# Kernel optimization log

Hardware: AMD Instinct MI355X
Metric: run time of the kernel (lower is better)

Reference implementation:

```python
import jax, jax.numpy as jnp
import numpy as np

B, T, F, H = 32, 512, 32, 256
EPS = 1e-5

def _ln(x, g, b):
    m = jnp.mean(x, axis=-1, keepdims=True)
    v = jnp.var(x, axis=-1, keepdims=True)
    return (x - m) / jnp.sqrt(v + EPS) * g + b

def setup_inputs() -> dict:
    key = jax.random.key(0)
    ks = jax.random.split(key, 30)
    n = lambda k, shp, fan: jax.random.normal(k, shp, dtype=jnp.float32) / np.sqrt(fan)
    d = {}
    d['x'] = jax.random.normal(ks[0], (B, T, F), dtype=jnp.float32)
    # per-feature GRN params (stacked over F); in_dim=1 so fc1/skip weights are (F,H)
    d['w1'] = n(ks[1], (F, H), 1); d['b1'] = jnp.zeros((F, H), jnp.float32)
    d['w2'] = n(ks[2], (F, H, H), H); d['b2'] = jnp.zeros((F, H), jnp.float32)
    d['wg'] = n(ks[3], (F, H, H), H); d['bg'] = jnp.zeros((F, H), jnp.float32)
    d['wf'] = n(ks[4], (F, H, H), H); d['bf'] = jnp.zeros((F, H), jnp.float32)
    d['gamma'] = jnp.ones((F, H), jnp.float32); d['beta'] = jnp.zeros((F, H), jnp.float32)
    d['ws'] = n(ks[5], (F, H), 1); d['bs'] = jnp.zeros((F, H), jnp.float32)
    # selection GRN: in_dim=F*H, hidden=H, out=F
    FH = F * H
    d['sw1'] = n(ks[6], (FH, H), FH); d['sb1'] = jnp.zeros((H,), jnp.float32)
    d['sw2'] = n(ks[7], (H, F), H); d['sb2'] = jnp.zeros((F,), jnp.float32)
    d['swg'] = n(ks[8], (F, F), F); d['sbg'] = jnp.zeros((F,), jnp.float32)
    d['swf'] = n(ks[9], (F, F), F); d['sbf'] = jnp.zeros((F,), jnp.float32)
    d['sgamma'] = jnp.ones((F,), jnp.float32); d['sbeta'] = jnp.zeros((F,), jnp.float32)
    d['ssw'] = n(ks[10], (FH, F), FH); d['ssb'] = jnp.zeros((F,), jnp.float32)
    return d

def reference(x, w1, b1, w2, b2, wg, bg, wf, bf, gamma, beta, ws, bs,
              sw1, sb1, sw2, sb2, swg, sbg, swf, sbf, sgamma, sbeta, ssw, ssb):
    # --- per-feature GRNs, vectorized over the feature axis ---
    xe = x[..., None]                                   # (B,T,F,1)
    h = jax.nn.elu(xe * w1 + b1)                        # (B,T,F,H)
    h = jnp.einsum('btfh,fhk->btfk', h, w2) + b2        # fc2
    glu = jax.nn.sigmoid(jnp.einsum('btfh,fhk->btfk', h, wg) + bg) \
          * (jnp.einsum('btfh,fhk->btfk', h, wf) + bf)
    residual = xe * ws + bs                             # skip Linear(1,H)
    stacked = _ln(residual + glu, gamma, beta)          # (B,T,F,H)
    # --- selection GRN over flattened features ---
    flat = stacked.reshape(B, T, F * H)
    sh = jax.nn.elu(flat @ sw1 + sb1)                   # (B,T,H)
    sh = sh @ sw2 + sb2                                 # (B,T,F)
    sglu = jax.nn.sigmoid(sh @ swg + sbg) * (sh @ swf + sbf)
    sres = flat @ ssw + ssb
    weights = jax.nn.softmax(_ln(sres + sglu, sgamma, sbeta), axis=-1)  # (B,T,F)
    # --- weighted sum over features ---
    return jnp.einsum('btfh,btf->bth', stacked, weights)  # (B,T,H)
```

## Files before the change

### kernel.cpp

```cpp
#include <hip/hip_runtime.h>
#include <hip/hip_bf16.h>
#include <hip/hip_fp16.h>

#define BT 16384
#define F 32
#define H 256
#define FH 8192
#define SPLITK 4

typedef _Float16 half8 __attribute__((ext_vector_type(8)));
typedef _Float16 half4v __attribute__((ext_vector_type(4)));
typedef float float4v __attribute__((ext_vector_type(4)));

#define GLD_LDS(gsrc, ldst) \
    __builtin_amdgcn_global_load_lds( \
        (const __attribute__((address_space(1))) void*)(gsrc), \
        (__attribute__((address_space(3))) void*)(ldst), 16, 0, 0)

#define WAITVM2_BAR() do { \
    __builtin_amdgcn_sched_barrier(0); \
    asm volatile("s_waitcnt vmcnt(2)" ::: "memory"); \
    __builtin_amdgcn_s_barrier(); \
    __builtin_amdgcn_sched_barrier(0); } while (0)
#define WAITVM0_BAR() do { \
    __builtin_amdgcn_sched_barrier(0); \
    asm volatile("s_waitcnt vmcnt(0)" ::: "memory"); \
    __builtin_amdgcn_s_barrier(); \
    __builtin_amdgcn_sched_barrier(0); } while (0)
#define END_BAR() do { \
    __builtin_amdgcn_sched_barrier(0); \
    __builtin_amdgcn_s_barrier(); \
    __builtin_amdgcn_sched_barrier(0); } while (0)
#define LGKM_BAR() do { \
    __builtin_amdgcn_sched_barrier(0); \
    asm volatile("s_waitcnt lgkmcnt(0)" ::: "memory"); \
    __builtin_amdgcn_s_barrier(); \
    __builtin_amdgcn_sched_barrier(0); } while (0)

__global__ __launch_bounds__(256) void transpose_w_kernel(
    const float* __restrict__ w2, const float* __restrict__ wg,
    const float* __restrict__ wf, _Float16* __restrict__ wt)
{
    __shared__ float tile[64][65];
    int bid = blockIdx.x;
    int tens = bid >> 9, rem = bid & 511;
    int f = rem >> 4, tl = rem & 15;
    int hb = (tl >> 2) * 64, nb = (tl & 3) * 64;
    const float* src = (tens == 0 ? w2 : (tens == 1 ? wg : wf)) + f * 65536;
    _Float16* dst = wt + (size_t)tens * 2097152 + f * 65536;
    int lane = threadIdx.x & 63, w = threadIdx.x >> 6;
    for (int i = 0; i < 16; ++i) {
        int r = i * 4 + w;
        tile[r][lane] = src[(hb + r) * 256 + nb + lane];
    }
    __syncthreads();
    for (int i = 0; i < 16; ++i) {
        int c = i * 4 + w;
        dst[(nb + c) * 256 + hb + lane] = (_Float16)tile[lane][c];
    }
}

__global__ __launch_bounds__(256) void transpose_s_kernel(
    const float* __restrict__ sw1, const float* __restrict__ ssw,
    _Float16* __restrict__ wcat)
{
    __shared__ float tile[64][65];
    int bid = blockIdx.x;
    int lane = threadIdx.x & 63, w = threadIdx.x >> 6;
    if (bid < 512) {
        int k0 = (bid >> 2) * 64, n0 = (bid & 3) * 64;
        for (int i = 0; i < 16; ++i) {
            int r = i * 4 + w;
            tile[r][lane] = sw1[(size_t)(k0 + r) * 256 + n0 + lane];
        }
        __syncthreads();
        for (int i = 0; i < 16; ++i) {
            int c = i * 4 + w;
            wcat[(size_t)(n0 + c) * FH + k0 + lane] = (_Float16)tile[lane][c];
        }
    } else {
        int k0 = (bid - 512) * 64;
        int t = threadIdx.x;
        for (int i = 0; i < 8; ++i) {
            int idx = t + i * 256;
            int r = idx >> 5, cc = idx & 31;
            tile[r][cc] = ssw[(size_t)(k0 + r) * 32 + cc];
        }
        __syncthreads();
        for (int i = 0; i < 8; ++i) {
            int idx = t + i * 256;
            int c = idx >> 6, rr = idx & 63;
            wcat[(size_t)(256 + c) * FH + k0 + rr] = (_Float16)tile[rr][c];
        }
    }
}

__global__ __launch_bounds__(512, 4) void grn_kernel(
    const float* __restrict__ x, const float* __restrict__ w1, const float* __restrict__ b1,
    const float* __restrict__ b2, const float* __restrict__ bg, const float* __restrict__ bfv_,
    const float* __restrict__ gamma, const float* __restrict__ beta,
    const float* __restrict__ wsk, const float* __restrict__ bsk,
    const _Float16* __restrict__ w2t, const _Float16* __restrict__ wgt,
    const _Float16* __restrict__ wft, _Float16* __restrict__ stacked, int tok_base)
{
    __shared__ __align__(16) char smem[65536];
    _Float16* As = (_Float16*)smem;
    _Float16* Bs = (_Float16*)(smem + 32768);
    float* red = (float*)smem;
    float* mv  = (float*)(smem + 2048);

    const int bid = blockIdx.x;
    const int xcd = bid & 7;
    const int slot = bid >> 3;
    const int f = xcd * 4 + (slot & 3);
    const int tok0 = (slot >> 2) * 64;
    const int t = threadIdx.x;
    const int wv = t >> 6;
    const int ln = t & 15;
    const int q  = (t >> 4) & 3;
    const int wm = wv >> 2;
    const int wn = wv & 3;
    const int r0 = wm * 32 + ln;
    const int r1 = r0 + 16;

    const _Float16* w2f = w2t + (size_t)f * 65536;
    const _Float16* wgf = wgt + (size_t)f * 65536;
    const _Float16* wff = wft + (size_t)f * 65536;

#define GRN_STAGE(buf, Bsrc, kc) do {                                          \
        const _Float16* _bp = (Bsrc);                                          \
        _Pragma("unroll")                                                      \
        for (int _i = 0; _i < 2; ++_i) {                                       \
            int _s = t + _i * 512;                                             \
            int _row = _s >> 2;                                                \
            int _c = (_s & 3) ^ ((_row >> 1) & 3);                             \
            GLD_LDS(_bp + _row * 256 + (kc) * 32 + _c * 8,                     \
                    Bs + (buf) * 8192 + _s * 8);                               \
        } } while (0)

#define GRN_MFMA(ACC, kc) do {                                                 \
        const _Float16* _B = Bs + ((kc) & 1) * 8192;                           \
        half8 _a0 = *(const half8*)&As[r0 * 256 + ((((kc) * 4 + q) ^ (r0 & 7)) << 3)]; \
        half8 _a1 = *(const half8*)&As[r1 * 256 + ((((kc) * 4 + q) ^ (r1 & 7)) << 3)]; \
        _Pragma("unroll")                                                      \
        for (int _nt = 0; _nt < 4; ++_nt) {                                    \
            int _rb = wn * 64 + _nt * 16 + ln;                                 \
            int _cp = q ^ ((_rb >> 1) & 3);                                    \
            half8 _b8 = *(const half8*)&_B[_rb * 32 + _cp * 8];                \
            ACC[0][_nt] = __builtin_amdgcn_mfma_f32_16x16x32_f16(              \
                _a0, _b8, ACC[0][_nt], 0, 0, 0);                               \
            ACC[1][_nt] = __builtin_amdgcn_mfma_f32_16x16x32_f16(              \
                _a1, _b8, ACC[1][_nt], 0, 0, 0);                               \
        } } while (0)

    float b2v[4];
#pragma unroll
    for (int nt = 0; nt < 4; ++nt) b2v[nt] = b2[f * H + wn * 64 + nt * 16 + ln];

    GRN_STAGE(0, w2f, 0);

    {
        const int colE = t & 255;
        const int rgE = __builtin_amdgcn_readfirstlane(t >> 8) * 32;
        const float w1v = w1[f * H + colE];
        const float b1v = b1[f * H + colE];
        const int chE = colE >> 3, elE = colE & 7;
#pragma unroll 8
        for (int i = 0; i < 32; ++i) {
            int row = rgE + i;
            float xv = x[(size_t)(tok_base + tok0 + row) * F + f];
            float z = fmaf(xv, w1v, b1v);
            float e = z > 0.f ? z : (__expf(z) - 1.f);
            As[row * 256 + ((chE ^ (row & 7)) << 3) + elE] = (_Float16)e;
        }
    }
    LGKM_BAR();

    float4v acc1[2][4];
#pragma unroll
    for (int mt = 0; mt < 2; ++mt)
#pragma unroll
        for (int nt = 0; nt < 4; ++nt)
#pragma unroll
            for (int r = 0; r < 4; ++r) acc1[mt][nt][r] = 0.f;

#pragma unroll
    for (int kc = 0; kc < 8; ++kc) {
        if (kc < 7) GRN_STAGE((kc + 1) & 1, w2f, kc + 1);
        else        GRN_STAGE(0, wgf, 0);
        WAITVM2_BAR();
        GRN_MFMA(acc1, kc);
        END_BAR();
    }

    {
#pragma unroll
        for (int mt = 0; mt < 2; ++mt)
#pragma unroll
            for (int nt = 0; nt < 4; ++nt) {
                int n = wn * 64 + nt * 16 + ln;
#pragma unroll
                for (int r = 0; r < 4; ++r) {
                    int row = wm * 32 + mt * 16 + q * 4 + r;
                    As[row * 256 + (((n >> 3) ^ (row & 7)) << 3) + (n & 7)] =
                        (_Float16)(acc1[mt][nt][r] + b2v[nt]);
                }
            }
    }
    LGKM_BAR();

    float4v accG[2][4], accF[2][4];
#pragma unroll
    for (int mt = 0; mt < 2; ++mt)
#pragma unroll
        for (int nt = 0; nt < 4; ++nt)
#pragma unroll
            for (int r = 0; r < 4; ++r) { accG[mt][nt][r] = 0.f; accF[mt][nt][r] = 0.f; }

#pragma unroll
    for (int kc = 0; kc < 8; ++kc) {
        if (kc < 7) GRN_STAGE((kc + 1) & 1, wgf, kc + 1);
        else        GRN_STAGE(0, wff, 0);
        WAITVM2_BAR();
        GRN_MFMA(accG, kc);
        END_BAR();
    }
#pragma unroll
    for (int kc = 0; kc < 8; ++kc) {
        if (kc < 7) {
            GRN_STAGE((kc + 1) & 1, wff, kc + 1);
            WAITVM2_BAR();
        } else {
            WAITVM0_BAR();
        }
        GRN_MFMA(accF, kc);
        END_BAR();
    }
#undef GRN_STAGE
#undef GRN_MFMA

    float xr[2][4];
#pragma unroll
    for (int mt = 0; mt < 2; ++mt)
#pragma unroll
        for (int r = 0; r < 4; ++r)
            xr[mt][r] = x[(size_t)(tok_base + tok0 + wm * 32 + mt * 16 + q * 4 + r) * F + f];
#pragma unroll
    for (int nt = 0; nt < 4; ++nt) {
        int nn = f * H + wn * 64 + nt * 16 + ln;
        float bgv = bg[nn], bfv = bfv_[nn], wsv = wsk[nn], bsv = bsk[nn];
#pragma unroll
        for (int mt = 0; mt < 2; ++mt)
#pragma unroll
            for (int r = 0; r < 4; ++r) {
                float cg = accG[mt][nt][r] + bgv;
                float cf = accF[mt][nt][r] + bfv;
                float sig = 1.f / (1.f + __expf(-cg));
                accG[mt][nt][r] = sig * cf + xr[mt][r] * wsv + bsv;
            }
    }

#pragma unroll
    for (int mt = 0; mt < 2; ++mt)
#pragma unroll
        for (int r = 0; r < 4; ++r) {
            float v0 = accG[mt][0][r], v1 = accG[mt][1][r];
            float v2 = accG[mt][2][r], v3 = accG[mt][3][r];
            float s1 = (v0 + v1) + (v2 + v3);
            float s2 = (v0 * v0 + v1 * v1) + (v2 * v2 + v3 * v3);
#pragma unroll
            for (int m = 1; m <= 8; m <<= 1) {
                s1 += __shfl_xor(s1, m, 64);
                s2 += __shfl_xor(s2, m, 64);
            }
            if (ln == 0) {
                int row = wm * 32 + mt * 16 + q * 4 + r;
                red[row * 4 + wn] = s1;
                red[256 + row * 4 + wn] = s2;
            }
        }
    __syncthreads();
    if (t < 64) {
        float a = (red[t * 4] + red[t * 4 + 1]) + (red[t * 4 + 2] + red[t * 4 + 3]);
        float b = (red[256 + t * 4] + red[256 + t * 4 + 1])
                + (red[256 + t * 4 + 2] + red[256 + t * 4 + 3]);
        float mean = a * (1.f / 256.f);
        float var = b * (1.f / 256.f) - mean * mean;
        mv[t] = mean;
        mv[64 + t] = rsqrtf(var + 1e-5f);
    }
    __syncthreads();

    float mr[2][4], rr[2][4];
#pragma unroll
    for (int mt = 0; mt < 2; ++mt)
#pragma unroll
        for (int r = 0; r < 4; ++r) {
            int row = wm * 32 + mt * 16 + q * 4 + r;
            mr[mt][r] = mv[row];
            rr[mt][r] = mv[64 + row];
        }
#pragma unroll
    for (int nt = 0; nt < 4; ++nt) {
        int n = wn * 64 + nt * 16 + ln;
        float gv = gamma[f * H + n], bvv = beta[f * H + n];
#pragma unroll
        for (int mt = 0; mt < 2; ++mt)
#pragma unroll
            for (int r = 0; r < 4; ++r) {
                int row = wm * 32 + mt * 16 + q * 4 + r;
                float vv = (accG[mt][nt][r] - mr[mt][r]) * rr[mt][r] * gv + bvv;
                stacked[(size_t)(tok0 + row) * FH + f * H + n] = (_Float16)vv;
            }
    }
}

__global__ __launch_bounds__(256, 3) void sel_gemm_kernel(
    const _Float16* __restrict__ stacked, const _Float16* __restrict__ wcat,
    float* __restrict__ sh_part, float* __restrict__ sres_part, int C)
{
    __shared__ __align__(16) _Float16 As2[2][64 * 64];
    const int t = threadIdx.x;
    const int wv = t >> 6;
    const int ln = t & 15, q = (t & 63) >> 4;
    const int bid = blockIdx.x;
    const int xcd = bid & 7;
    const int slot = bid >> 3;
    const int kb = xcd >> 1;
    const int tok0 = (slot * 2 + (xcd & 1)) * 64;

    const int s1 = t + 256;
    const int row0 = t >> 3,  c0 = ((t & 7) ^ (row0 & 7)) * 8;
    const int row1 = s1 >> 3, c1 = ((s1 & 7) ^ (row1 & 7)) * 8;
    const _Float16* a0src = stacked + (size_t)(tok0 + row0) * FH + kb * 2048 + c0;
    const _Float16* a1src = stacked + (size_t)(tok0 + row1) * FH + kb * 2048 + c1;

    float4v acc[4][5];
#pragma unroll
    for (int mt = 0; mt < 4; ++mt)
#pragma unroll
        for (int i = 0; i < 5; ++i)
#pragma unroll
            for (int r = 0; r < 4; ++r) acc[mt][i][r] = 0.f;

    GLD_LDS(a0src, &As2[0][t * 8]);
    GLD_LDS(a1src, &As2[0][s1 * 8]);
    __syncthreads();

    for (int kc = 0; kc < 32; ++kc) {
        const int cur = kc & 1;
        half8 bb0[5], bb1[5];
#define SEL_LOAD(i)                                                            \
        {                                                                      \
            const _Float16* bp = wcat                                          \
                + (size_t)((wv + 4 * (i)) * 16 + ln) * FH                      \
                + kb * 2048 + kc * 64 + q * 8;                                 \
            bb0[i] = *(const half8*)bp;                                        \
            bb1[i] = *(const half8*)(bp + 32);                                 \
        }
        SEL_LOAD(0) SEL_LOAD(1) SEL_LOAD(2) SEL_LOAD(3)
        if (wv < 2) SEL_LOAD(4)
#undef SEL_LOAD
        if (kc < 31) {
            GLD_LDS(a0src + (kc + 1) * 64, &As2[cur ^ 1][t * 8]);
            GLD_LDS(a1src + (kc + 1) * 64, &As2[cur ^ 1][s1 * 8]);
        }
        const _Float16* As = As2[cur];
        half8 af0[4], af1[4];
#pragma unroll
        for (int mt = 0; mt < 4; ++mt) {
            int row = mt * 16 + ln;
            af0[mt] = *(const half8*)&As[row * 64 + ((q ^ (row & 7)) * 8)];
            af1[mt] = *(const half8*)&As[row * 64 + (((4 + q) ^ (row & 7)) * 8)];
        }
#define SEL_FMA(i)                                                            \
        {                                                                      \
            _Pragma("unroll")                                                  \
            for (int mt = 0; mt < 4; ++mt)                                     \
                acc[mt][i] = __builtin_amdgcn_mfma_f32_16x16x32_f16(           \
                    af0[mt], bb0[i], acc[mt][i], 0, 0, 0);                     \
            _Pragma("unroll")                                                  \
            for (int mt = 0; mt < 4; ++mt)                                     \
                acc[mt][i] = __builtin_amdgcn_mfma_f32_16x16x32_f16(           \
                    af1[mt], bb1[i], acc[mt][i], 0, 0, 0);                     \
        }
        SEL_FMA(0) SEL_FMA(1) SEL_FMA(2) SEL_FMA(3)
        if (wv < 2) SEL_FMA(4)
#undef SEL_FMA
        __syncthreads();
    }

    float* shp = sh_part + (size_t)kb * ((size_t)C * 256);
    float* srp = sres_part + (size_t)kb * ((size_t)C * 32);
#pragma unroll
    for (int i = 0; i < 4; ++i) {
        int n = (wv + 4 * i) * 16 + ln;
#pragma unroll
        for (int mt = 0; mt < 4; ++mt)
#pragma unroll
            for (int r = 0; r < 4; ++r) {
                int m = tok0 + mt * 16 + q * 4 + r;
                shp[(size_t)m * 256 + n] = acc[mt][i][r];
            }
    }
    if (wv < 2) {
        int n = wv * 16 + ln;
#pragma unroll
        for (int mt = 0; mt < 4; ++mt)
#pragma unroll
            for (int r = 0; r < 4; ++r) {
                int m = tok0 + mt * 16 + q * 4 + r;
                srp[(size_t)m * 32 + n] = acc[mt][4][r];
            }
    }
}

__global__ __launch_bounds__(256) void tail_kernel(
    const float* __restrict__ sh_part, const float* __restrict__ sres_part,
    const _Float16* __restrict__ stacked,
    const float* __restrict__ sb1, const float* __restrict__ ssb,
    const float* __restrict__ sw2, const float* __restrict__ sb2,
    const float* __restrict__ swg, const float* __restrict__ sbg,
    const float* __restrict__ swf, const float* __restrict__ sbf,
    const float* __restrict__ sgam, const float* __restrict__ sbet,
    float* __restrict__ out, int tok_base, int C)
{
    __shared__ float sw2s[256 * 32];
    __shared__ float swgs[1024], swfs[1024];
    __shared__ float shv[8][260];
    __shared__ float wls[8][33];
    const int t = threadIdx.x;
    const size_t shS = (size_t)C * 256;
    const size_t srS = (size_t)C * 32;
    for (int i = 0; i < 32; ++i) sw2s[t + i * 256] = sw2[t + i * 256];
    for (int i = 0; i < 4; ++i) {
        swgs[t + i * 256] = swg[t + i * 256];
        swfs[t + i * 256] = swf[t + i * 256];
    }
#pragma unroll
    for (int i = 0; i < 2; ++i) {
        int slot = t + i * 256;
        int gg = slot >> 6;
        int c4 = (slot & 63) * 4;
        size_t o = (size_t)(blockIdx.x * 8 + gg) * 256 + c4;
        float4v z = *(const float4v*)&sb1[c4];
        z += *(const float4v*)&sh_part[o];
        z += *(const float4v*)&sh_part[shS + o];
        z += *(const float4v*)&sh_part[2 * shS + o];
        z += *(const float4v*)&sh_part[3 * shS + o];
        float4v e;
#pragma unroll
        for (int j = 0; j < 4; ++j)
            e[j] = z[j] > 0.f ? z[j] : (__expf(z[j]) - 1.f);
        *(float4v*)&shv[gg][c4] = e;
    }
    __syncthreads();
    const int g = t >> 5;
    const int j = t & 31;
    const int token = blockIdx.x * 8 + g;
    float p = sb2[j];
    for (int k = 0; k < 256; ++k) p += shv[g][k] * sw2s[k * 32 + j];
    float gacc = sbg[j], uacc = sbf[j];
#pragma unroll 8
    for (int i = 0; i < 32; ++i) {
        float tv = __shfl(p, i, 32);
        gacc += tv * swgs[i * 32 + j];
        uacc += tv * swfs[i * 32 + j];
    }
    float sig = 1.f / (1.f + __expf(-gacc));
    size_t o2 = (size_t)token * 32 + j;
    float sresv = ssb[j] + sres_part[o2] + sres_part[srS + o2]
                + sres_part[2 * srS + o2] + sres_part[3 * srS + o2];
    float sv = sresv + sig * uacc;
    float s1 = sv, s2 = sv * sv;
    for (int off = 16; off; off >>= 1) {
        s1 += __shfl_xor(s1, off, 32);
        s2 += __shfl_xor(s2, off, 32);
    }
    float mean = s1 * (1.f / 32.f);
    float var = s2 * (1.f / 32.f) - mean * mean;
    float v = (sv - mean) * rsqrtf(var + 1e-5f) * sgam[j] + sbet[j];
    float mx = v;
    for (int off = 16; off; off >>= 1) mx = fmaxf(mx, __shfl_xor(mx, off, 32));
    float e = __expf(v - mx);
    float ssum = e;
    for (int off = 16; off; off >>= 1) ssum += __shfl_xor(ssum, off, 32);
    wls[g][j] = e / ssum;
    __syncthreads();
    {
        const int tg = t >> 6;
        const int c4 = (t & 63) * 4;
#pragma unroll
        for (int tt = 0; tt < 2; ++tt) {
            int tk = tg * 2 + tt;
            const _Float16* sp = stacked + (size_t)(blockIdx.x * 8 + tk) * FH;
            float a0 = 0.f, a1 = 0.f, a2 = 0.f, a3 = 0.f;
#pragma unroll
            for (int f = 0; f < 32; ++f) {
                half4v vv = *(const half4v*)&sp[f * 256 + c4];
                float w = wls[tk][f];
                a0 += (float)vv[0] * w;
                a1 += (float)vv[1] * w;
                a2 += (float)vv[2] * w;
                a3 += (float)vv[3] * w;
            }
            float4v ov; ov[0] = a0; ov[1] = a1; ov[2] = a2; ov[3] = a3;
            *(float4v*)&out[(size_t)(tok_base + blockIdx.x * 8 + tk) * 256 + c4] = ov;
        }
    }
}

extern "C" void kernel_launch(void* const* d_in, const int* in_sizes, int n_in,
                              void* d_out, int out_size, void* d_ws, size_t ws_size,
                              hipStream_t stream)
{
    (void)in_sizes; (void)n_in; (void)out_size;
    const float* x    = (const float*)d_in[0];
    const float* w1   = (const float*)d_in[1];
    const float* b1   = (const float*)d_in[2];
    const float* w2   = (const float*)d_in[3];
    const float* b2   = (const float*)d_in[4];
    const float* wg   = (const float*)d_in[5];
    const float* bg   = (const float*)d_in[6];
    const float* wf   = (const float*)d_in[7];
    const float* bfp  = (const float*)d_in[8];
    const float* gamma= (const float*)d_in[9];
    const float* beta = (const float*)d_in[10];
    const float* wsk  = (const float*)d_in[11];
    const float* bsk  = (const float*)d_in[12];
    const float* sw1  = (const float*)d_in[13];
    const float* sb1  = (const float*)d_in[14];
    const float* sw2  = (const float*)d_in[15];
    const float* sb2  = (const float*)d_in[16];
    const float* swg  = (const float*)d_in[17];
    const float* sbg  = (const float*)d_in[18];
    const float* swf  = (const float*)d_in[19];
    const float* sbf  = (const float*)d_in[20];
    const float* sgam = (const float*)d_in[21];
    const float* sbet = (const float*)d_in[22];
    const float* ssw  = (const float*)d_in[23];
    const float* ssb  = (const float*)d_in[24];

    const size_t fixedB = 12582912 + 4718592;
    int C = BT;
    while (C > 512) {
        size_t need = fixedB + (size_t)C * 20992;
        if (need <= ws_size) break;
        C >>= 1;
    }
    const int nChunks = BT / C;

    char* ws = (char*)d_ws;
    _Float16* wt      = (_Float16*)ws;
    _Float16* wcat    = (_Float16*)(ws + 12582912);
    char* p = ws + fixedB;
    _Float16* stacked = (_Float16*)p;            p += (size_t)C * FH * 2;
    float* sh_part    = (float*)p;               p += (size_t)C * 256 * 4 * SPLITK;
    float* sres_part  = (float*)p;
    float* out        = (float*)d_out;

    hipLaunchKernelGGL(transpose_w_kernel, dim3(1536), dim3(256), 0, stream, w2, wg, wf, wt);
    hipLaunchKernelGGL(transpose_s_kernel, dim3(640), dim3(256), 0, stream, sw1, ssw, wcat);
    for (int c = 0; c < nChunks; ++c) {
        int tb = c * C;
        hipLaunchKernelGGL(grn_kernel, dim3((C / 64) * 32), dim3(512), 0, stream,
                           x, w1, b1, b2, bg, bfp, gamma, beta, wsk, bsk,
                           wt, wt + 2097152, wt + 2 * 2097152, stacked, tb);
        hipLaunchKernelGGL(sel_gemm_kernel, dim3((C / 64) * SPLITK), dim3(256), 0, stream,
                           stacked, wcat, sh_part, sres_part, C);
        hipLaunchKernelGGL(tail_kernel, dim3(C / 8), dim3(256), 0, stream,
                           sh_part, sres_part, stacked, sb1, ssb, sw2, sb2, swg, sbg, swf, sbf,
                           sgam, sbet, out, tb, C);
    }
}
```

Before: 716.6 us.

## Triple-buffer GRN weight tiles with prefetch distance two and one barrier per step

Weight tiles staged into LDS go from double buffering to a three-slot ring. Each step now issues the load two tiles ahead and runs behind a single barrier, where before it needed a wait barrier and an end barrier. The step index runs continuously across the fc2, gate and fc matmuls, so prefetch flows across the phase boundaries. The goal is to hide global-to-LDS latency and cut barrier stalls, at the cost of 16 KB more shared memory per block, which could affect occupancy.

```diff
diff --git a/kernel.cpp b/kernel.cpp
--- a/kernel.cpp
+++ b/kernel.cpp
@@ -103,7 +103,7 @@
     const _Float16* __restrict__ w2t, const _Float16* __restrict__ wgt,
     const _Float16* __restrict__ wft, _Float16* __restrict__ stacked, int tok_base)
 {
-    __shared__ __align__(16) char smem[65536];
+    __shared__ __align__(16) char smem[81920];
     _Float16* As = (_Float16*)smem;
     _Float16* Bs = (_Float16*)(smem + 32768);
     float* red = (float*)smem;
@@ -138,10 +138,11 @@
                     Bs + (buf) * 8192 + _s * 8);                               \
         } } while (0)
 
-#define GRN_MFMA(ACC, kc) do {                                                 \
-        const _Float16* _B = Bs + ((kc) & 1) * 8192;                           \
-        half8 _a0 = *(const half8*)&As[r0 * 256 + ((((kc) * 4 + q) ^ (r0 & 7)) << 3)]; \
-        half8 _a1 = *(const half8*)&As[r1 * 256 + ((((kc) * 4 + q) ^ (r1 & 7)) << 3)]; \
+#define GRN_MFMA(ACC, s) do {                                                  \
+        const _Float16* _B = Bs + ((s) % 3) * 8192;                            \
+        const int _kc = (s) & 7;                                               \
+        half8 _a0 = *(const half8*)&As[r0 * 256 + (((_kc * 4 + q) ^ (r0 & 7)) << 3)]; \
+        half8 _a1 = *(const half8*)&As[r1 * 256 + (((_kc * 4 + q) ^ (r1 & 7)) << 3)]; \
         _Pragma("unroll")                                                      \
         for (int _nt = 0; _nt < 4; ++_nt) {                                    \
             int _rb = wn * 64 + _nt * 16 + ln;                                 \
@@ -174,6 +175,7 @@
             As[row * 256 + ((chE ^ (row & 7)) << 3) + elE] = (_Float16)e;
         }
     }
+    GRN_STAGE(1, w2f, 1);
     LGKM_BAR();
 
     float4v acc1[2][4];
@@ -185,13 +187,13 @@
             for (int r = 0; r < 4; ++r) acc1[mt][nt][r] = 0.f;
 
 #pragma unroll
-    for (int kc = 0; kc < 8; ++kc) {
-        if (kc < 7) GRN_STAGE((kc + 1) & 1, w2f, kc + 1);
-        else        GRN_STAGE(0, wgf, 0);
+    for (int s = 0; s < 8; ++s) {
         WAITVM2_BAR();
-        GRN_MFMA(acc1, kc);
-        END_BAR();
-    }
+        if (s < 6) GRN_STAGE((s + 2) % 3, w2f, s + 2);
+        else       GRN_STAGE((s + 2) % 3, wgf, s - 6);
+        GRN_MFMA(acc1, s);
+    }
+    END_BAR();
 
     {
 #pragma unroll
@@ -218,24 +220,21 @@
             for (int r = 0; r < 4; ++r) { accG[mt][nt][r] = 0.f; accF[mt][nt][r] = 0.f; }
 
 #pragma unroll
-    for (int kc = 0; kc < 8; ++kc) {
-        if (kc < 7) GRN_STAGE((kc + 1) & 1, wgf, kc + 1);
-        else        GRN_STAGE(0, wff, 0);
+    for (int s8 = 0; s8 < 8; ++s8) {
+        const int s = s8 + 8;
         WAITVM2_BAR();
-        GRN_MFMA(accG, kc);
-        END_BAR();
-    }
-#pragma unroll
-    for (int kc = 0; kc < 8; ++kc) {
-        if (kc < 7) {
-            GRN_STAGE((kc + 1) & 1, wff, kc + 1);
-            WAITVM2_BAR();
-        } else {
-            WAITVM0_BAR();
-        }
-        GRN_MFMA(accF, kc);
-        END_BAR();
-    }
+        if (s8 < 6) GRN_STAGE((s + 2) % 3, wgf, s8 + 2);
+        else        GRN_STAGE((s + 2) % 3, wff, s8 - 6);
+        GRN_MFMA(accG, s);
+    }
+#pragma unroll
+    for (int s8 = 0; s8 < 8; ++s8) {
+        const int s = s8 + 16;
+        if (s8 < 7) { WAITVM2_BAR(); } else { WAITVM0_BAR(); }
+        if (s8 < 6) GRN_STAGE((s + 2) % 3, wff, s8 + 2);
+        GRN_MFMA(accF, s);
+    }
+    END_BAR();
 #undef GRN_STAGE
 #undef GRN_MFMA
 
```

Result: faster. 700.1 us (-2.3%).
